# Performance work log

Measured on AMD Instinct MI355X. Metric: run time of the kernel, lower is better.

The kernel has to match this reference:

```python
import jax, jax.numpy as jnp
import numpy as np

N_NODES = 50000
N_EDGES = 800000
NODE_DIM = 128
EDGE_IN = 31
EMB_DIM = 128
GATE_HID = 128
INIT_GATE_BIAS = 2.0


def setup_inputs() -> dict:
    key = jax.random.key(0)
    ks = jax.random.split(key, 8)
    x = jax.random.normal(ks[0], (N_NODES, NODE_DIM), dtype=jnp.float32)
    edge_attr = jax.random.normal(ks[1], (N_EDGES, EDGE_IN), dtype=jnp.float32)
    edge_index = jax.random.randint(ks[2], (2, N_EDGES), 0, N_NODES, dtype=jnp.int64)
    gate_in_dim = 2 * NODE_DIM + EDGE_IN
    # params (torch.nn.Linear-style scaled uniform init)
    def lin(k, fan_in, fan_out):
        bound = 1.0 / np.sqrt(fan_in)
        kw, kb = jax.random.split(k)
        W = jax.random.uniform(kw, (fan_in, fan_out), minval=-bound, maxval=bound, dtype=jnp.float32)
        b = jax.random.uniform(kb, (fan_out,), minval=-bound, maxval=bound, dtype=jnp.float32)
        return W, b
    W_proj, b_proj = lin(ks[3], EDGE_IN, EMB_DIM)
    W1, b1 = lin(ks[4], gate_in_dim, GATE_HID)
    W2, _ = lin(ks[5], GATE_HID, 1)
    b2 = jnp.full((1,), INIT_GATE_BIAS, dtype=jnp.float32)
    return {
        "x": x,
        "edge_attr": edge_attr,
        "edge_index": edge_index,
        "W_proj": W_proj,
        "b_proj": b_proj,
        "W1": W1,
        "b1": b1,
        "W2": W2,
        "b2": b2,
    }


def reference(x, edge_attr, edge_index, W_proj, b_proj, W1, b1, W2, b2):
    src = edge_index[0]
    dst = edge_index[1]
    xu = x[src]                      # [E, node_dim] gather
    xv = x[dst]                      # [E, node_dim] gather
    base = edge_attr @ W_proj + b_proj            # [E, emb_dim]
    gate_in = jnp.concatenate([xu, xv, edge_attr], axis=-1)  # [E, 2*node_dim+31]
    h = jax.nn.gelu(gate_in @ W1 + b1)            # [E, gate_hidden]
    gate = jax.nn.sigmoid(h @ W2 + b2)            # [E, 1]
    return base * gate                            # [E, emb_dim]
```

## Files before the change

### kernel.cpp

```cpp
#include <hip/hip_runtime.h>
#include <math.h>

#define N_NODES 50000
#define N_EDGES 800000

typedef __attribute__((ext_vector_type(8))) short bf16x8;
typedef __attribute__((ext_vector_type(4))) float f32x4;

__device__ __forceinline__ unsigned f2bfu(float f) {
  union { float f; unsigned u; } v; v.f = f;
  return (v.u + 0x7FFFu + ((v.u >> 16) & 1u)) >> 16;
}
__device__ __forceinline__ short f2bf(float f) { return (short)f2bfu(f); }

__device__ __forceinline__ float bflo(unsigned d) {
  union { unsigned u; float f; } v; v.u = d << 16; return v.f;
}
__device__ __forceinline__ float bfhi(unsigned d) {
  union { unsigned u; float f; } v; v.u = d & 0xFFFF0000u; return v.f;
}

__device__ __forceinline__ float gelu_f(float h) {
  const float m1 = h * h;
  const float t2u = h * fmaf(0.07135481f, m1, 1.5957691f);
  const float e = __expf(t2u);
  const float rc = __builtin_amdgcn_rcpf(1.f + e);
  return h - h * rc;
}

#define PIN(v) asm volatile("" : "+v"(v))

__global__ void wfrag_kernel(const float* __restrict__ W_proj,
                             const float* __restrict__ W1,
                             const float* __restrict__ b_proj,
                             uint4* __restrict__ wfrag) {
  const int id = threadIdx.x;
  const int mat = id >> 9;
  const int fid = id & 511;
  const int mb = fid >> 6, ln = fid & 63;
  const int rr = ln & 15, gg = ln >> 4;
  const float* W = mat ? W_proj : (W1 + (size_t)256 * 128);
  union { uint4 u; bf16x8 b; } f;
#pragma unroll
  for (int t = 0; t < 8; ++t) {
    const int kk = gg * 8 + t;
    float v = 0.f;
    if (kk < 31) v = W[(size_t)kk * 128 + 16 * mb + rr];
    else if (mat == 1 && kk == 31) v = b_proj[16 * mb + rr];
    f.b[t] = f2bf(v);
  }
  wfrag[id] = f.u;
}

__global__ __launch_bounds__(256) void node_kernel(
    const float* __restrict__ x, const float* __restrict__ W1,
    const float* __restrict__ b1, unsigned short* __restrict__ AB) {
  const int l = threadIdx.x & 63;
  const int wv = threadIdx.x >> 6;
  const int r = l & 15, g4 = l >> 4;

  const int wid = blockIdx.x * 4 + wv;
  const int s = wid & 3;

  bf16x8 wA[4][4];
#pragma unroll
  for (int q = 0; q < 4; ++q) {
    const int c = 16 * (4 * s + q) + r;
    const float* Wb = (c < 128) ? (W1 + c) : (W1 + 128 * 128 + (c - 128));
#pragma unroll
    for (int ks = 0; ks < 4; ++ks) {
#pragma unroll
      for (int t = 0; t < 8; ++t)
        wA[q][ks][t] = f2bf(Wb[(size_t)(ks * 32 + g4 * 8 + t) * 128]);
      PIN(wA[q][ks]);
    }
  }
  float4 bv[4];
#pragma unroll
  for (int q = 0; q < 4; ++q)
    bv[q] = *(const float4*)(b1 + ((16 * (4 * s + q) + g4 * 4) & 127));

  const int half = s >> 1;

  for (int t0 = wid >> 2; t0 < (N_NODES / 16); t0 += 1024) {
    const int n0 = t0 * 16;
    f32x4 acc[4] = {{0,0,0,0},{0,0,0,0},{0,0,0,0},{0,0,0,0}};
#pragma unroll
    for (int ks = 0; ks < 4; ++ks) {
      const float* xr = x + (size_t)(n0 + r) * 128 + ks * 32 + g4 * 8;
      const float4 x0 = *(const float4*)xr;
      const float4 x1 = *(const float4*)(xr + 4);
      bf16x8 xb;
      xb[0] = f2bf(x0.x); xb[1] = f2bf(x0.y); xb[2] = f2bf(x0.z); xb[3] = f2bf(x0.w);
      xb[4] = f2bf(x1.x); xb[5] = f2bf(x1.y); xb[6] = f2bf(x1.z); xb[7] = f2bf(x1.w);
#pragma unroll
      for (int q = 0; q < 4; ++q)
        acc[q] = __builtin_amdgcn_mfma_f32_16x16x32_bf16(wA[q][ks], xb, acc[q], 0, 0, 0);
    }
#pragma unroll
    for (int q = 0; q < 4; ++q) {
      const int mb8 = 4 * (s & 1) + q;
      const float o0 = acc[q][0] + 0.5f * bv[q].x;
      const float o1 = acc[q][1] + 0.5f * bv[q].y;
      const float o2 = acc[q][2] + 0.5f * bv[q].z;
      const float o3 = acc[q][3] + 0.5f * bv[q].w;
      uint2 pk;
      pk.x = f2bfu(o0) | (f2bfu(o1) << 16);
      pk.y = f2bfu(o2) | (f2bfu(o3) << 16);
      *(uint2*)(AB + (size_t)(n0 + r) * 256 + half * 128 + g4 * 32 + mb8 * 4) = pk;
    }
  }
}

__global__ __launch_bounds__(256) void edge_kernel(
    const float* __restrict__ edge_attr, const int* __restrict__ edge_index,
    const unsigned short* __restrict__ AB, const uint4* __restrict__ wfrag,
    const float* __restrict__ W2, const float* __restrict__ b2,
    float* __restrict__ out) {
  __shared__ float tlds[4][16 * 128];
  __shared__ uint4 wPl[512];
  const int tid = threadIdx.x;
  const int l = tid & 63;
  const int wv = tid >> 6;
  const int r = l & 15, g4 = l >> 4;
  float* const tl = &tlds[wv][0];

  wPl[tid] = wfrag[512 + tid];
  wPl[tid + 256] = wfrag[768 + tid];

  bf16x8 wH[8];
#pragma unroll
  for (int mb = 0; mb < 8; ++mb) {
    union { uint4 u; bf16x8 b; } h;
    h.u = wfrag[mb * 64 + l];
    wH[mb] = h.b;
    PIN(wH[mb]);
  }
  const float b2v = b2[0];
  __syncthreads();

  const int nwaves = gridDim.x * 4;
  const int NT = N_EDGES / 16;

  int tile = blockIdx.x * 4 + wv;
  if (tile >= NT) return;

  int sA, dA;
  uint4 ua[4], ub[4];
  float ear[8];
  {
    const int e = tile * 16 + r;
    const int cs = edge_index[e];
    const int cd = edge_index[N_EDGES + e];
    const uint4* ap4 = (const uint4*)(AB + (size_t)cs * 256 + g4 * 32);
    const uint4* bp4 = (const uint4*)(AB + (size_t)cd * 256 + 128 + g4 * 32);
#pragma unroll
    for (int t = 0; t < 4; ++t) { ua[t] = ap4[t]; ub[t] = bp4[t]; }
    const float* earp = edge_attr + (size_t)e * 31 + g4 * 8;
#pragma unroll
    for (int t = 0; t < 8; ++t)
      ear[t] = (g4 * 8 + t < 31) ? earp[t] : 0.f;
    const int tn = tile + nwaves;
    const int en = (tn < NT ? tn : tile) * 16 + r;
    sA = edge_index[en];
    dA = edge_index[N_EDGES + en];
  }

  for (; tile < NT; tile += nwaves) {
    const int tn = tile + nwaves;
    const int tn2 = tile + 2 * nwaves;

    const int en2 = (tn2 < NT ? tn2 : tile) * 16 + r;
    const int sB = edge_index[en2];
    const int dB = edge_index[N_EDGES + en2];

    bf16x8 eb;
#pragma unroll
    for (int t = 0; t < 8; ++t) eb[t] = f2bf(ear[t]);
    if (g4 == 3) eb[7] = (short)0x3F80;

    f32x4 acch[8];
#pragma unroll
    for (int t = 0; t < 4; ++t) {
      acch[2 * t][0]     = bflo(ua[t].x) + bflo(ub[t].x);
      acch[2 * t][1]     = bfhi(ua[t].x) + bfhi(ub[t].x);
      acch[2 * t][2]     = bflo(ua[t].y) + bflo(ub[t].y);
      acch[2 * t][3]     = bfhi(ua[t].y) + bfhi(ub[t].y);
      acch[2 * t + 1][0] = bflo(ua[t].z) + bflo(ub[t].z);
      acch[2 * t + 1][1] = bfhi(ua[t].z) + bfhi(ub[t].z);
      acch[2 * t + 1][2] = bflo(ua[t].w) + bflo(ub[t].w);
      acch[2 * t + 1][3] = bfhi(ua[t].w) + bfhi(ub[t].w);
    }

    if (tn < NT) {
      const uint4* ap4 = (const uint4*)(AB + (size_t)sA * 256 + g4 * 32);
      const uint4* bp4 = (const uint4*)(AB + (size_t)dA * 256 + 128 + g4 * 32);
#pragma unroll
      for (int t = 0; t < 4; ++t) { ua[t] = ap4[t]; ub[t] = bp4[t]; }
      const float* earp = edge_attr + (size_t)(tn * 16 + r) * 31 + g4 * 8;
#pragma unroll
      for (int t = 0; t < 8; ++t)
        if (g4 * 8 + t < 31) ear[t] = earp[t];
    }

#pragma unroll
    for (int mb = 0; mb < 8; ++mb)
      acch[mb] = __builtin_amdgcn_mfma_f32_16x16x32_bf16(wH[mb], eb, acch[mb], 0, 0, 0);

    float lg = 0.f;
#pragma unroll
    for (int mb = 0; mb < 8; ++mb) {
      const float4 w2v = *(const float4*)(W2 + 16 * mb + 4 * g4);
      lg = fmaf(gelu_f(acch[mb][0]), w2v.x, lg);
      lg = fmaf(gelu_f(acch[mb][1]), w2v.y, lg);
      lg = fmaf(gelu_f(acch[mb][2]), w2v.z, lg);
      lg = fmaf(gelu_f(acch[mb][3]), w2v.w, lg);
    }
    lg += __shfl_xor(lg, 16);
    lg += __shfl_xor(lg, 32);
    const float gate = __builtin_amdgcn_rcpf(1.f + __expf(-(lg + b2v)));

    unsigned zoff = 0;
    PIN(zoff);

#pragma unroll
    for (int mb = 0; mb < 8; ++mb) {
      union { uint4 u; bf16x8 b; } wp;
      wp.u = wPl[mb * 64 + l + zoff];
      f32x4 ac = __builtin_amdgcn_mfma_f32_16x16x32_bf16(
          wp.b, eb, (f32x4){0.f, 0.f, 0.f, 0.f}, 0, 0, 0);
      f32x4 o;
      o[0] = ac[0] * gate;
      o[1] = ac[1] * gate;
      o[2] = ac[2] * gate;
      o[3] = ac[3] * gate;
      const int col = 16 * mb + 4 * g4;
      *(f32x4*)(tl + 128 * r + (col ^ ((r & 7) << 2))) = o;
    }

    float* const obase = out + (size_t)tile * 16 * 128;
#pragma unroll
    for (int k = 0; k < 8; ++k) {
      const int row = 2 * k + (l >> 5);
      const int col = 4 * (l & 31);
      const f32x4 v = *(const f32x4*)(tl + 128 * row + (col ^ ((row & 7) << 2)));
      __builtin_nontemporal_store(v, (f32x4*)(obase + 256 * k + 4 * l));
    }

    sA = sB; dA = dB;
  }
}

extern "C" void kernel_launch(void* const* d_in, const int* in_sizes, int n_in,
                              void* d_out, int out_size, void* d_ws, size_t ws_size,
                              hipStream_t stream) {
  const float* x          = (const float*)d_in[0];
  const float* edge_attr  = (const float*)d_in[1];
  const int*   edge_index = (const int*)d_in[2];
  const float* W_proj     = (const float*)d_in[3];
  const float* b_proj     = (const float*)d_in[4];
  const float* W1         = (const float*)d_in[5];
  const float* b1         = (const float*)d_in[6];
  const float* W2         = (const float*)d_in[7];
  const float* b2         = (const float*)d_in[8];
  float* out = (float*)d_out;
  unsigned short* AB = (unsigned short*)d_ws;
  uint4* wfrag = (uint4*)(AB + (size_t)N_NODES * 256);

  hipLaunchKernelGGL(wfrag_kernel, dim3(1), dim3(1024), 0, stream,
                     W_proj, W1, b_proj, wfrag);
  hipLaunchKernelGGL(node_kernel, dim3(1024), dim3(256), 0, stream,
                     x, W1, b1, AB);
  hipLaunchKernelGGL(edge_kernel, dim3(2048), dim3(256), 0, stream,
                     edge_attr, edge_index, AB, wfrag, W2, b2,
                     out);
}
```

Baseline: 171.4 us.

## Stage node rows in LDS, fold log2e into GELU/sigmoid exp2, halve edge grid

In the node kernel, each block now loads a 16-row tile of x once into shared memory, and its four waves read that tile for their column slices. Before, each wave re-read the same rows from global memory. The GELU and sigmoid exponentials now call exp2f with the log2(e) factor folded into the constants, removing a multiply per exp. The edge kernel grid is halved from 2048 to 1024 blocks. The shared-memory staging adds two barriers per tile, and the smaller edge grid changes occupancy and per-block work.

```diff
diff --git a/kernel.cpp b/kernel.cpp
--- a/kernel.cpp
+++ b/kernel.cpp
@@ -22,8 +22,8 @@
 
 __device__ __forceinline__ float gelu_f(float h) {
   const float m1 = h * h;
-  const float t2u = h * fmaf(0.07135481f, m1, 1.5957691f);
-  const float e = __expf(t2u);
+  const float a = h * fmaf(0.10295276f, m1, 2.30231120f);
+  const float e = exp2f(a);
   const float rc = __builtin_amdgcn_rcpf(1.f + e);
   return h - h * rc;
 }
@@ -55,13 +55,13 @@
 __global__ __launch_bounds__(256) void node_kernel(
     const float* __restrict__ x, const float* __restrict__ W1,
     const float* __restrict__ b1, unsigned short* __restrict__ AB) {
-  const int l = threadIdx.x & 63;
-  const int wv = threadIdx.x >> 6;
+  __shared__ float xs[16 * 132];
+  const int tid = threadIdx.x;
+  const int l = tid & 63;
+  const int wv = tid >> 6;
   const int r = l & 15, g4 = l >> 4;
 
-  const int wid = blockIdx.x * 4 + wv;
-  const int s = wid & 3;
-
+  const int s = wv;
   bf16x8 wA[4][4];
 #pragma unroll
   for (int q = 0; q < 4; ++q) {
@@ -81,21 +81,29 @@
     bv[q] = *(const float4*)(b1 + ((16 * (4 * s + q) + g4 * 4) & 127));
 
   const int half = s >> 1;
-
-  for (int t0 = wid >> 2; t0 < (N_NODES / 16); t0 += 1024) {
+  const int srow = tid >> 4, scol = (tid & 15) * 8;
+
+  for (int t0 = blockIdx.x; t0 < (N_NODES / 16); t0 += gridDim.x) {
     const int n0 = t0 * 16;
+    const float4 xa = *(const float4*)(x + (size_t)(n0 + srow) * 128 + scol);
+    const float4 xb4 = *(const float4*)(x + (size_t)(n0 + srow) * 128 + scol + 4);
+    __syncthreads();
+    *(float4*)(xs + srow * 132 + scol) = xa;
+    *(float4*)(xs + srow * 132 + scol + 4) = xb4;
+    __syncthreads();
+
     f32x4 acc[4] = {{0,0,0,0},{0,0,0,0},{0,0,0,0},{0,0,0,0}};
 #pragma unroll
     for (int ks = 0; ks < 4; ++ks) {
-      const float* xr = x + (size_t)(n0 + r) * 128 + ks * 32 + g4 * 8;
+      const float* xr = xs + r * 132 + ks * 32 + g4 * 8;
       const float4 x0 = *(const float4*)xr;
       const float4 x1 = *(const float4*)(xr + 4);
-      bf16x8 xb;
-      xb[0] = f2bf(x0.x); xb[1] = f2bf(x0.y); xb[2] = f2bf(x0.z); xb[3] = f2bf(x0.w);
-      xb[4] = f2bf(x1.x); xb[5] = f2bf(x1.y); xb[6] = f2bf(x1.z); xb[7] = f2bf(x1.w);
+      bf16x8 xv;
+      xv[0] = f2bf(x0.x); xv[1] = f2bf(x0.y); xv[2] = f2bf(x0.z); xv[3] = f2bf(x0.w);
+      xv[4] = f2bf(x1.x); xv[5] = f2bf(x1.y); xv[6] = f2bf(x1.z); xv[7] = f2bf(x1.w);
 #pragma unroll
       for (int q = 0; q < 4; ++q)
-        acc[q] = __builtin_amdgcn_mfma_f32_16x16x32_bf16(wA[q][ks], xb, acc[q], 0, 0, 0);
+        acc[q] = __builtin_amdgcn_mfma_f32_16x16x32_bf16(wA[q][ks], xv, acc[q], 0, 0, 0);
     }
 #pragma unroll
     for (int q = 0; q < 4; ++q) {
@@ -218,7 +226,8 @@
     }
     lg += __shfl_xor(lg, 16);
     lg += __shfl_xor(lg, 32);
-    const float gate = __builtin_amdgcn_rcpf(1.f + __expf(-(lg + b2v)));
+    const float gate =
+        __builtin_amdgcn_rcpf(1.f + exp2f(-1.44269504f * (lg + b2v)));
 
     unsigned zoff = 0;
     PIN(zoff);
@@ -271,7 +280,7 @@
                      W_proj, W1, b_proj, wfrag);
   hipLaunchKernelGGL(node_kernel, dim3(1024), dim3(256), 0, stream,
                      x, W1, b1, AB);
-  hipLaunchKernelGGL(edge_kernel, dim3(2048), dim3(256), 0, stream,
+  hipLaunchKernelGGL(edge_kernel, dim3(1024), dim3(256), 0, stream,
                      edge_attr, edge_index, AB, wfrag, W2, b2,
                      out);
 }
```

Result: faster. 166.3 us (-3.0%).
